# Performance work log

Measured on AMD Instinct MI355X. Metric: run time of the kernel, lower is better.

Reference implementation:

```python
import jax, jax.numpy as jnp
import numpy as np

N_NODES = 100000
N_EDGES = 1600000
N_GRAPHS = 1000
F_IN, HID = 9, 64


def _glorot(key, shape):
    fan_in, fan_out = shape[0], shape[1]
    lim = (6.0 / (fan_in + fan_out)) ** 0.5
    return jax.random.uniform(key, shape, jnp.float32, -lim, lim)


def setup_inputs() -> dict:
    key = jax.random.key(0)
    ks = jax.random.split(key, 12)
    x = jax.random.normal(ks[0], (N_NODES, F_IN), jnp.float32)
    edge_index = jax.random.randint(ks[1], (2, N_EDGES), 0, N_NODES, jnp.int64)
    edge_attr = jnp.zeros((N_EDGES, 1), jnp.float32)
    batch = jnp.sort(jax.random.randint(ks[2], (N_NODES,), 0, N_GRAPHS, jnp.int64))
    # SAGEConv layer 1: 9 -> 64 (lin_l on aggregated neighbors w/ bias, lin_r on root)
    Wl1 = _glorot(ks[3], (F_IN, HID)); Wr1 = _glorot(ks[4], (F_IN, HID)); b1 = jnp.zeros((HID,), jnp.float32)
    # SAGEConv layer 2: 64 -> 64
    Wl2 = _glorot(ks[5], (HID, HID)); Wr2 = _glorot(ks[6], (HID, HID)); b2 = jnp.zeros((HID,), jnp.float32)
    # MLP readout: 64 -> 32 -> 1
    Wm1 = _glorot(ks[7], (HID, HID // 2)); bm1 = jnp.zeros((HID // 2,), jnp.float32)
    Wm2 = _glorot(ks[8], (HID // 2, 1)); bm2 = jnp.zeros((1,), jnp.float32)
    return dict(x=x, edge_index=edge_index, edge_attr=edge_attr, batch=batch,
                Wl1=Wl1, Wr1=Wr1, b1=b1, Wl2=Wl2, Wr2=Wr2, b2=b2,
                Wm1=Wm1, bm1=bm1, Wm2=Wm2, bm2=bm2)


def _sage_conv(x, src, dst, Wl, Wr, b, n_nodes):
    # mean aggregation of source-node features onto target nodes
    msgs = x[src]                                              # [E, F] gather
    s = jax.ops.segment_sum(msgs, dst, num_segments=n_nodes)   # [N, F] scatter-add
    cnt = jax.ops.segment_sum(jnp.ones((src.shape[0],), x.dtype), dst, num_segments=n_nodes)
    agg = s / jnp.maximum(cnt, 1.0)[:, None]
    return agg @ Wl + x @ Wr + b


def reference(x, edge_index, edge_attr, batch,
              Wl1, Wr1, b1, Wl2, Wr2, b2, Wm1, bm1, Wm2, bm2):
    src, dst = edge_index[0], edge_index[1]
    n = x.shape[0]
    h = jax.nn.relu(_sage_conv(x, src, dst, Wl1, Wr1, b1, n))
    h = _sage_conv(h, src, dst, Wl2, Wr2, b2, n)               # no act after last layer
    # global mean pool over graphs
    gs = jax.ops.segment_sum(h, batch, num_segments=N_GRAPHS)
    gc = jax.ops.segment_sum(jnp.ones((n,), h.dtype), batch, num_segments=N_GRAPHS)
    xg = gs / jnp.maximum(gc, 1.0)[:, None]                    # [G, 64]
    out = jax.nn.sigmoid(jax.nn.relu(xg @ Wm1 + bm1) @ Wm2 + bm2)  # [G, 1]
    return out
```

## Files before the change

### kernel.cpp

```cpp
#include <hip/hip_runtime.h>
#include <math.h>

#define N_NODES  100000
#define N_EDGES  1600000
#define N_GRAPHS 1000
#define F_IN     9
#define HID      64
#define NBUCK    196
#define BCAP     12288
#define CHUNK    4096

typedef unsigned int uint32;
typedef float v2f __attribute__((ext_vector_type(2)));


__device__ __forceinline__ uint32 pk_lo(float a, float b, uint32 old) {
    return (uint32)__builtin_amdgcn_cvt_pk_fp8_f32(a, b, (int)old, false);
}
__device__ __forceinline__ uint32 pk_hi(float a, float b, uint32 old) {
    return (uint32)__builtin_amdgcn_cvt_pk_fp8_f32(a, b, (int)old, true);
}

__global__ __launch_bounds__(256) void pad_part_kernel(const float* __restrict__ x,
                                                       const int* __restrict__ ei,
                                                       int* __restrict__ gcur,
                                                       int* __restrict__ ebuf,
                                                       uint32* __restrict__ x8b) {
    __shared__ int lcnt[NBUCK], lbase[NBUCK];
    int tid = threadIdx.x;

    int n = blockIdx.x * 256 + tid;
    if (n < N_NODES) {
        uint32 w[4];
        #pragma unroll
        for (int p = 0; p < 4; ++p) {
            float v0 = (4 * p + 0 < F_IN) ? x[(size_t)n * F_IN + 4 * p + 0] : 0.0f;
            float v1 = (4 * p + 1 < F_IN) ? x[(size_t)n * F_IN + 4 * p + 1] : 0.0f;
            float v2 = (4 * p + 2 < F_IN) ? x[(size_t)n * F_IN + 4 * p + 2] : 0.0f;
            float v3 = (4 * p + 3 < F_IN) ? x[(size_t)n * F_IN + 4 * p + 3] : 0.0f;
            w[p] = pk_hi(v2, v3, pk_lo(v0, v1, 0u));
        }
        *reinterpret_cast<uint4*>(&x8b[(size_t)n * 4]) =
            make_uint4(w[0], w[1], w[2], w[3]);
    }

    for (int i = tid; i < NBUCK; i += 256) lcnt[i] = 0;
    __syncthreads();
    int e0 = blockIdx.x * CHUNK;
    int e1 = e0 + CHUNK; if (e1 > N_EDGES) e1 = N_EDGES;
    for (int e = e0 + tid; e < e1; e += 256)
        atomicAdd(&lcnt[ei[N_EDGES + e] >> 9], 1);
    __syncthreads();
    for (int i = tid; i < NBUCK; i += 256)
        lbase[i] = atomicAdd(&gcur[i], lcnt[i]);
    __syncthreads();
    for (int i = tid; i < NBUCK; i += 256) lcnt[i] = 0;
    __syncthreads();
    for (int e = e0 + tid; e < e1; e += 256) {
        int src = ei[e];
        int dst = ei[N_EDGES + e];
        int b = dst >> 9;
        int pos = lbase[b] + atomicAdd(&lcnt[b], 1);
        if (pos < BCAP)
            ebuf[(size_t)b * BCAP + pos] = src | ((dst & 511) << 17);
    }
}

__global__ __launch_bounds__(512) void build_csr_kernel(const int* __restrict__ ebuf,
                                                        const int* __restrict__ gcur,
                                                        int2* __restrict__ rowcnt,
                                                        int* __restrict__ col) {
    __shared__ int cnt[512];
    __shared__ int cur[512];
    __shared__ int wsum[8];
    int b = blockIdx.x;
    int n0 = b << 9;
    int tid = threadIdx.x;
    int ec = gcur[b]; if (ec > BCAP) ec = BCAP;
    size_t base = (size_t)b * BCAP;
    cnt[tid] = 0;
    __syncthreads();
    for (int e = tid; e < ec; e += 512)
        atomicAdd(&cnt[(uint32)ebuf[base + e] >> 17], 1);
    __syncthreads();
    int v = cnt[tid];
    int lane = tid & 63, wid = tid >> 6;
    int s = v;
    #pragma unroll
    for (int off = 1; off < 64; off <<= 1) {
        int u = __shfl_up(s, off, 64);
        if (lane >= off) s += u;
    }
    if (lane == 63) wsum[wid] = s;
    __syncthreads();
    int add = 0;
    for (int w = 0; w < wid; ++w) add += wsum[w];
    int off_ex = s - v + add;
    int n = n0 + tid;
    if (n < N_NODES) rowcnt[n] = make_int2((int)base + off_ex, v);
    cur[tid] = off_ex;
    __syncthreads();
    for (int e = tid; e < ec; e += 512) {
        int pv = ebuf[base + e];
        int pos = atomicAdd(&cur[(uint32)pv >> 17], 1);
        col[base + pos] = pv & 0x1FFFF;
    }
}

__global__ __launch_bounds__(256) void agg_l1_kernel(const float* __restrict__ x,
                                                     const uint32* __restrict__ x8b,
                                                     const int2* __restrict__ rowcnt,
                                                     const int* __restrict__ col,
                                                     const float* __restrict__ Wl1,
                                                     const float* __restrict__ Wr1,
                                                     const float* __restrict__ b1,
                                                     const int* __restrict__ batch,
                                                     uint32* __restrict__ h1b,
                                                     float* __restrict__ poolH) {
    __shared__ float w1s[F_IN * 128];
    __shared__ float bs[HID];
    __shared__ float ss[64 * 17];
    __shared__ float xs[64 * 10];
    __shared__ float hs[64 * 65];
    int tid = threadIdx.x;
    int n0 = blockIdx.x * 64;
    for (int i = tid; i < F_IN * HID; i += 256) {
        int f = i >> 6, j = i & 63;
        w1s[f * 128 + j]      = Wl1[i];
        w1s[f * 128 + 64 + j] = Wr1[i];
    }
    if (tid < HID) bs[tid] = b1[tid];
    for (int i = tid; i < 64 * F_IN; i += 256) {
        int r = i / F_IN, f = i - r * F_IN;
        int n = n0 + r;
        xs[r * 10 + f] = (n < N_NODES) ? x[(size_t)n * F_IN + f] : 0.0f;
    }

    {
        int r = tid >> 2, q = tid & 3;
        int n = n0 + r;
        v2f a01 = {0.f, 0.f}, a23 = {0.f, 0.f};
        int deg = 0;
        if (n < N_NODES) {
            int2 rc = rowcnt[n];
            deg = rc.y;
            int i = 0;
            for (; i + 1 < deg; i += 2) {
                int c0 = col[rc.x + i];
                int c1 = col[rc.x + i + 1];
                uint32 d0 = x8b[(size_t)c0 * 4 + q];
                uint32 d1 = x8b[(size_t)c1 * 4 + q];
                a01 += __builtin_amdgcn_cvt_pk_f32_fp8((int)d0, false);
                a23 += __builtin_amdgcn_cvt_pk_f32_fp8((int)d0, true);
                a01 += __builtin_amdgcn_cvt_pk_f32_fp8((int)d1, false);
                a23 += __builtin_amdgcn_cvt_pk_f32_fp8((int)d1, true);
            }
            if (i < deg) {
                uint32 d0 = x8b[(size_t)col[rc.x + i] * 4 + q];
                a01 += __builtin_amdgcn_cvt_pk_f32_fp8((int)d0, false);
                a23 += __builtin_amdgcn_cvt_pk_f32_fp8((int)d0, true);
            }
        }
        float inv = 1.0f / fmaxf((float)deg, 1.0f);
        int q4 = q * 4;
        ss[r * 17 + q4 + 0] = a01[0] * inv;
        ss[r * 17 + q4 + 1] = a01[1] * inv;
        ss[r * 17 + q4 + 2] = a23[0] * inv;
        ss[r * 17 + q4 + 3] = a23[1] * inv;
    }
    __syncthreads();

    int r = tid >> 2, cg = tid & 3, k0 = cg * 16;
    float h[16];
    #pragma unroll
    for (int kk = 0; kk < 16; ++kk) {
        int k = k0 + kk;
        float v = bs[k];
        #pragma unroll
        for (int f = 0; f < F_IN; ++f)
            v += ss[r * 17 + f] * w1s[f * 128 + k]
               + xs[r * 10 + f] * w1s[f * 128 + 64 + k];
        v = fmaxf(v, 0.0f);
        h[kk] = v;
        hs[r * 65 + k] = v;
    }
    int n = n0 + r;
    if (n < N_NODES) {
        uint32 w[4];
        #pragma unroll
        for (int p = 0; p < 4; ++p)
            w[p] = pk_hi(h[4 * p + 2], h[4 * p + 3],
                         pk_lo(h[4 * p + 0], h[4 * p + 1], 0u));
        *reinterpret_cast<uint4*>(&h1b[(size_t)n * 16 + cg * 4]) =
            make_uint4(w[0], w[1], w[2], w[3]);
    }
    __syncthreads();
    if (tid < HID) {
        int j = tid;
        int cur = batch[(n0 < N_NODES) ? n0 : (N_NODES - 1)];
        float v = (n0 < N_NODES) ? hs[0 * 65 + j] : 0.0f;
        for (int rr = 1; rr < 64; ++rr) {
            int nn = n0 + rr;
            bool ok = (nn < N_NODES);
            int g = batch[ok ? nn : (N_NODES - 1)];
            float val = ok ? hs[rr * 65 + j] : 0.0f;
            if (g == cur) v += val;
            else { atomicAdd(&poolH[cur * HID + j], v); cur = g; v = val; }
        }
        atomicAdd(&poolH[cur * HID + j], v);
    }
}

__global__ __launch_bounds__(256) void gather2_kernel(const uint32* __restrict__ h1b,
                                                      const int2* __restrict__ rowcnt,
                                                      const int* __restrict__ col,
                                                      const int* __restrict__ batch,
                                                      float* __restrict__ poolA) {
    __shared__ float sh[4][HID];
    int w = threadIdx.x >> 6;
    int lane = threadIdx.x & 63;
    int slot = lane >> 3;
    int grp  = lane & 7;
    int n = blockIdx.x * 4 + w;
    int2 rc = rowcnt[n];
    const uint32* hb = h1b + grp * 2;
    v2f a0 = {0.f, 0.f}, a1 = {0.f, 0.f}, a2 = {0.f, 0.f}, a3 = {0.f, 0.f};
    int i = rc.x + slot;
    int end = rc.x + rc.y;
    for (; i + 8 < end; i += 16) {
        int c0 = col[i];
        int c1 = col[i + 8];
        uint2 d0 = *reinterpret_cast<const uint2*>(hb + (size_t)c0 * 16);
        uint2 d1 = *reinterpret_cast<const uint2*>(hb + (size_t)c1 * 16);
        a0 += __builtin_amdgcn_cvt_pk_f32_fp8((int)d0.x, false);
        a1 += __builtin_amdgcn_cvt_pk_f32_fp8((int)d0.x, true);
        a2 += __builtin_amdgcn_cvt_pk_f32_fp8((int)d0.y, false);
        a3 += __builtin_amdgcn_cvt_pk_f32_fp8((int)d0.y, true);
        a0 += __builtin_amdgcn_cvt_pk_f32_fp8((int)d1.x, false);
        a1 += __builtin_amdgcn_cvt_pk_f32_fp8((int)d1.x, true);
        a2 += __builtin_amdgcn_cvt_pk_f32_fp8((int)d1.y, false);
        a3 += __builtin_amdgcn_cvt_pk_f32_fp8((int)d1.y, true);
    }
    if (i < end) {
        int c0 = col[i];
        uint2 d0 = *reinterpret_cast<const uint2*>(hb + (size_t)c0 * 16);
        a0 += __builtin_amdgcn_cvt_pk_f32_fp8((int)d0.x, false);
        a1 += __builtin_amdgcn_cvt_pk_f32_fp8((int)d0.x, true);
        a2 += __builtin_amdgcn_cvt_pk_f32_fp8((int)d0.y, false);
        a3 += __builtin_amdgcn_cvt_pk_f32_fp8((int)d0.y, true);
    }
    float r8[8] = {a0[0], a0[1], a1[0], a1[1], a2[0], a2[1], a3[0], a3[1]};
    #pragma unroll
    for (int k = 0; k < 8; ++k) {
        r8[k] += __shfl_xor(r8[k], 8, 64);
        r8[k] += __shfl_xor(r8[k], 16, 64);
        r8[k] += __shfl_xor(r8[k], 32, 64);
    }
    float inv = 1.0f / fmaxf((float)rc.y, 1.0f);
    if (slot == 0) {
        #pragma unroll
        for (int k = 0; k < 8; ++k)
            sh[w][grp * 8 + k] = r8[k] * inv;
    }
    __syncthreads();
    if (threadIdx.x < HID) {
        int j = threadIdx.x;
        int base = blockIdx.x * 4;
        int cur = batch[base];
        float v = sh[0][j];
        #pragma unroll
        for (int r = 1; r < 4; ++r) {
            int g = batch[base + r];
            float val = sh[r][j];
            if (g == cur) v += val;
            else { atomicAdd(&poolA[cur * HID + j], v); cur = g; v = val; }
        }
        atomicAdd(&poolA[cur * HID + j], v);
    }
}

__global__ void mlp_kernel(const float* __restrict__ poolA,
                           const float* __restrict__ poolH,
                           const int* __restrict__ batch,
                           const float* __restrict__ Wl2,
                           const float* __restrict__ Wr2,
                           const float* __restrict__ b2,
                           const float* __restrict__ Wm1,
                           const float* __restrict__ bm1,
                           const float* __restrict__ Wm2,
                           const float* __restrict__ bm2,
                           float* __restrict__ out) {
    __shared__ float spA[4][HID], spH[4][HID], sx[4][HID];
    int t = blockIdx.x * blockDim.x + threadIdx.x;
    int g = t >> 6;
    int j = t & 63;
    int w = threadIdx.x >> 6;
    if (g >= N_GRAPHS) return;
    int lo = 0, hi = N_NODES;
    while (lo < hi) { int m = (lo + hi) >> 1; if (batch[m] < g) lo = m + 1; else hi = m; }
    int start = lo;
    lo = 0; hi = N_NODES;
    while (lo < hi) { int m = (lo + hi) >> 1; if (batch[m] < g + 1) lo = m + 1; else hi = m; }
    int cntg = lo - start;
    float inv = 1.0f / fmaxf((float)cntg, 1.0f);
    spA[w][j] = poolA[g * HID + j];
    spH[w][j] = poolH[g * HID + j];
    float acc = 0.0f;
    #pragma unroll 8
    for (int k = 0; k < HID; ++k)
        acc += spA[w][k] * Wl2[k * HID + j] + spH[w][k] * Wr2[k * HID + j];
    sx[w][j] = acc * inv + b2[j];
    if (j < 32) {
        float a = bm1[j];
        #pragma unroll 8
        for (int k = 0; k < HID; ++k)
            a += sx[w][k] * Wm1[k * 32 + j];
        float r = fmaxf(a, 0.0f) * Wm2[j];
        #pragma unroll
        for (int off = 16; off > 0; off >>= 1)
            r += __shfl_down(r, off, 32);
        if (j == 0)
            out[g] = 1.0f / (1.0f + expf(-(r + bm2[0])));
    }
}

extern "C" void kernel_launch(void* const* d_in, const int* in_sizes, int n_in,
                              void* d_out, int out_size, void* d_ws, size_t ws_size,
                              hipStream_t stream) {
    const float* x    = (const float*)d_in[0];
    const int*   ei   = (const int*)d_in[1];
    const int*   batch= (const int*)d_in[3];
    const float* Wl1  = (const float*)d_in[4];
    const float* Wr1  = (const float*)d_in[5];
    const float* b1   = (const float*)d_in[6];
    const float* Wl2  = (const float*)d_in[7];
    const float* Wr2  = (const float*)d_in[8];
    const float* b2   = (const float*)d_in[9];
    const float* Wm1  = (const float*)d_in[10];
    const float* bm1  = (const float*)d_in[11];
    const float* Wm2  = (const float*)d_in[12];
    const float* bm2  = (const float*)d_in[13];
    float* out = (float*)d_out;

    int*   wsi = (int*)d_ws;
    float* wsf = (float*)d_ws;
    float*  poolA  = wsf;
    float*  poolH  = wsf + 64000;
    int*    gcur   = wsi + 128000;
    int2*   rowcnt = (int2*)(wsi + 128200);
    int*    col    = wsi + 328200;
    int*    ebuf   = wsi + 2736648;
    uint32* x8b    = (uint32*)(wsi + 5145096);
    uint32* h1b    = (uint32*)(wsi + 5545096);

    hipMemsetAsync(d_ws, 0, 128200 * sizeof(int), stream);

    {   int bl = (N_EDGES + CHUNK - 1) / CHUNK;
        pad_part_kernel<<<bl, 256, 0, stream>>>(x, ei, gcur, ebuf, x8b);
    }
    build_csr_kernel<<<NBUCK, 512, 0, stream>>>(ebuf, gcur, rowcnt, col);
    {   int th = 256, bl = (N_NODES + 63) / 64;
        agg_l1_kernel<<<bl, th, 0, stream>>>(x, x8b, rowcnt, col, Wl1, Wr1, b1,
                                             batch, h1b, poolH);
    }
    {   int th = 256, bl = N_NODES / 4;
        gather2_kernel<<<bl, th, 0, stream>>>(h1b, rowcnt, col, batch, poolA);
    }
    {   int th = 256, bl = (N_GRAPHS * 64) / th;
        mlp_kernel<<<bl, th, 0, stream>>>(poolA, poolH, batch,
                                          Wl2, Wr2, b2, Wm1, bm1, Wm2, bm2, out);
    }
}
```

Baseline: 139.4 us.

## Split layer-1 gather into wave-per-node kernel and halve CSR bucket size

The layer-1 neighbour gather moves out of the fused aggregation kernel into a separate kernel. There, one 64-lane wave handles each node, 16 slots stride over its edges and a shuffle reduction combines them, writing mean features to a new s16 buffer. The dense layer-1 kernel then only loads those sums. CSR construction buckets become 256 nodes instead of 512, doubling the number of build blocks for more parallelism, with the workspace layout adjusted. The cost is an extra launch and an extra round trip of the intermediate buffer through global memory. Halving bucket capacity to 6144 raises the risk of overflow on skewed inputs.

Result: slower. 152.9 us (+9.7%).

```diff
diff --git a/kernel.cpp b/kernel.cpp
--- a/kernel.cpp
+++ b/kernel.cpp
@@ -6,8 +6,8 @@
 #define N_GRAPHS 1000
 #define F_IN     9
 #define HID      64
-#define NBUCK    196
-#define BCAP     12288
+#define NBUCK    391
+#define BCAP     6144
 #define CHUNK    4096
 
 typedef unsigned int uint32;
@@ -49,7 +49,7 @@
     int e0 = blockIdx.x * CHUNK;
     int e1 = e0 + CHUNK; if (e1 > N_EDGES) e1 = N_EDGES;
     for (int e = e0 + tid; e < e1; e += 256)
-        atomicAdd(&lcnt[ei[N_EDGES + e] >> 9], 1);
+        atomicAdd(&lcnt[ei[N_EDGES + e] >> 8], 1);
     __syncthreads();
     for (int i = tid; i < NBUCK; i += 256)
         lbase[i] = atomicAdd(&gcur[i], lcnt[i]);
@@ -59,10 +59,10 @@
     for (int e = e0 + tid; e < e1; e += 256) {
         int src = ei[e];
         int dst = ei[N_EDGES + e];
-        int b = dst >> 9;
+        int b = dst >> 8;
         int pos = lbase[b] + atomicAdd(&lcnt[b], 1);
         if (pos < BCAP)
-            ebuf[(size_t)b * BCAP + pos] = src | ((dst & 511) << 17);
+            ebuf[(size_t)b * BCAP + pos] = src | ((dst & 255) << 17);
     }
 }
 
@@ -70,35 +70,40 @@
                                                         const int* __restrict__ gcur,
                                                         int2* __restrict__ rowcnt,
                                                         int* __restrict__ col) {
-    __shared__ int cnt[512];
-    __shared__ int cur[512];
-    __shared__ int wsum[8];
+    __shared__ int cnt[256];
+    __shared__ int cur[256];
+    __shared__ int wsum[4];
     int b = blockIdx.x;
-    int n0 = b << 9;
+    int n0 = b << 8;
     int tid = threadIdx.x;
     int ec = gcur[b]; if (ec > BCAP) ec = BCAP;
     size_t base = (size_t)b * BCAP;
-    cnt[tid] = 0;
+    if (tid < 256) cnt[tid] = 0;
     __syncthreads();
     for (int e = tid; e < ec; e += 512)
         atomicAdd(&cnt[(uint32)ebuf[base + e] >> 17], 1);
     __syncthreads();
-    int v = cnt[tid];
+    int v = 0, s = 0;
     int lane = tid & 63, wid = tid >> 6;
-    int s = v;
-    #pragma unroll
-    for (int off = 1; off < 64; off <<= 1) {
-        int u = __shfl_up(s, off, 64);
-        if (lane >= off) s += u;
-    }
-    if (lane == 63) wsum[wid] = s;
-    __syncthreads();
-    int add = 0;
-    for (int w = 0; w < wid; ++w) add += wsum[w];
-    int off_ex = s - v + add;
-    int n = n0 + tid;
-    if (n < N_NODES) rowcnt[n] = make_int2((int)base + off_ex, v);
-    cur[tid] = off_ex;
+    if (tid < 256) {
+        v = cnt[tid];
+        s = v;
+        #pragma unroll
+        for (int off = 1; off < 64; off <<= 1) {
+            int u = __shfl_up(s, off, 64);
+            if (lane >= off) s += u;
+        }
+        if (lane == 63) wsum[wid] = s;
+    }
+    __syncthreads();
+    if (tid < 256) {
+        int add = 0;
+        for (int w = 0; w < wid; ++w) add += wsum[w];
+        int off_ex = s - v + add;
+        int n = n0 + tid;
+        if (n < N_NODES) rowcnt[n] = make_int2((int)base + off_ex, v);
+        cur[tid] = off_ex;
+    }
     __syncthreads();
     for (int e = tid; e < ec; e += 512) {
         int pv = ebuf[base + e];
@@ -107,16 +112,46 @@
     }
 }
 
-__global__ __launch_bounds__(256) void agg_l1_kernel(const float* __restrict__ x,
-                                                     const uint32* __restrict__ x8b,
-                                                     const int2* __restrict__ rowcnt,
-                                                     const int* __restrict__ col,
-                                                     const float* __restrict__ Wl1,
-                                                     const float* __restrict__ Wr1,
-                                                     const float* __restrict__ b1,
-                                                     const int* __restrict__ batch,
-                                                     uint32* __restrict__ h1b,
-                                                     float* __restrict__ poolH) {
+__global__ __launch_bounds__(256) void gather1_kernel(const uint32* __restrict__ x8b,
+                                                      const int2* __restrict__ rowcnt,
+                                                      const int* __restrict__ col,
+                                                      float* __restrict__ s16) {
+    int w = threadIdx.x >> 6;
+    int lane = threadIdx.x & 63;
+    int slot = lane >> 2;
+    int q    = lane & 3;
+    int n = blockIdx.x * 4 + w;
+    int2 rc = rowcnt[n];
+    v2f a01 = {0.f, 0.f}, a23 = {0.f, 0.f};
+    for (int i = slot; i < rc.y; i += 16) {
+        int c = col[rc.x + i];
+        uint32 d = x8b[(size_t)c * 4 + q];
+        a01 += __builtin_amdgcn_cvt_pk_f32_fp8((int)d, false);
+        a23 += __builtin_amdgcn_cvt_pk_f32_fp8((int)d, true);
+    }
+    float r4[4] = {a01[0], a01[1], a23[0], a23[1]};
+    #pragma unroll
+    for (int k = 0; k < 4; ++k) {
+        r4[k] += __shfl_xor(r4[k], 4, 64);
+        r4[k] += __shfl_xor(r4[k], 8, 64);
+        r4[k] += __shfl_xor(r4[k], 16, 64);
+        r4[k] += __shfl_xor(r4[k], 32, 64);
+    }
+    if (slot == 0) {
+        float inv = 1.0f / fmaxf((float)rc.y, 1.0f);
+        *reinterpret_cast<float4*>(&s16[(size_t)n * 16 + q * 4]) =
+            make_float4(r4[0] * inv, r4[1] * inv, r4[2] * inv, r4[3] * inv);
+    }
+}
+
+__global__ __launch_bounds__(256) void l1_kernel(const float* __restrict__ x,
+                                                 const float* __restrict__ s16,
+                                                 const float* __restrict__ Wl1,
+                                                 const float* __restrict__ Wr1,
+                                                 const float* __restrict__ b1,
+                                                 const int* __restrict__ batch,
+                                                 uint32* __restrict__ h1b,
+                                                 float* __restrict__ poolH) {
     __shared__ float w1s[F_IN * 128];
     __shared__ float bs[HID];
     __shared__ float ss[64 * 17];
@@ -130,43 +165,15 @@
         w1s[f * 128 + 64 + j] = Wr1[i];
     }
     if (tid < HID) bs[tid] = b1[tid];
+    for (int i = tid; i < 64 * 16; i += 256) {
+        int r = i >> 4, f = i & 15;
+        int n = n0 + r;
+        ss[r * 17 + f] = (n < N_NODES) ? s16[(size_t)n * 16 + f] : 0.0f;
+    }
     for (int i = tid; i < 64 * F_IN; i += 256) {
         int r = i / F_IN, f = i - r * F_IN;
         int n = n0 + r;
         xs[r * 10 + f] = (n < N_NODES) ? x[(size_t)n * F_IN + f] : 0.0f;
-    }
-
-    {
-        int r = tid >> 2, q = tid & 3;
-        int n = n0 + r;
-        v2f a01 = {0.f, 0.f}, a23 = {0.f, 0.f};
-        int deg = 0;
-        if (n < N_NODES) {
-            int2 rc = rowcnt[n];
-            deg = rc.y;
-            int i = 0;
-            for (; i + 1 < deg; i += 2) {
-                int c0 = col[rc.x + i];
-                int c1 = col[rc.x + i + 1];
-                uint32 d0 = x8b[(size_t)c0 * 4 + q];
-                uint32 d1 = x8b[(size_t)c1 * 4 + q];
-                a01 += __builtin_amdgcn_cvt_pk_f32_fp8((int)d0, false);
-                a23 += __builtin_amdgcn_cvt_pk_f32_fp8((int)d0, true);
-                a01 += __builtin_amdgcn_cvt_pk_f32_fp8((int)d1, false);
-                a23 += __builtin_amdgcn_cvt_pk_f32_fp8((int)d1, true);
-            }
-            if (i < deg) {
-                uint32 d0 = x8b[(size_t)col[rc.x + i] * 4 + q];
-                a01 += __builtin_amdgcn_cvt_pk_f32_fp8((int)d0, false);
-                a23 += __builtin_amdgcn_cvt_pk_f32_fp8((int)d0, true);
-            }
-        }
-        float inv = 1.0f / fmaxf((float)deg, 1.0f);
-        int q4 = q * 4;
-        ss[r * 17 + q4 + 0] = a01[0] * inv;
-        ss[r * 17 + q4 + 1] = a01[1] * inv;
-        ss[r * 17 + q4 + 2] = a23[0] * inv;
-        ss[r * 17 + q4 + 3] = a23[1] * inv;
     }
     __syncthreads();
 
@@ -347,21 +354,24 @@
     float*  poolA  = wsf;
     float*  poolH  = wsf + 64000;
     int*    gcur   = wsi + 128000;
-    int2*   rowcnt = (int2*)(wsi + 128200);
-    int*    col    = wsi + 328200;
-    int*    ebuf   = wsi + 2736648;
-    uint32* x8b    = (uint32*)(wsi + 5145096);
-    uint32* h1b    = (uint32*)(wsi + 5545096);
-
-    hipMemsetAsync(d_ws, 0, 128200 * sizeof(int), stream);
+    int2*   rowcnt = (int2*)(wsi + 128400);
+    int*    col    = wsi + 328400;
+    int*    ebuf   = wsi + 2730704;
+    uint32* x8b    = (uint32*)(wsi + 5133008);
+    float*  s16    = wsf + 5533008;
+    uint32* h1b    = (uint32*)(wsi + 7133008);
+
+    hipMemsetAsync(d_ws, 0, 128400 * sizeof(int), stream);
 
     {   int bl = (N_EDGES + CHUNK - 1) / CHUNK;
         pad_part_kernel<<<bl, 256, 0, stream>>>(x, ei, gcur, ebuf, x8b);
     }
     build_csr_kernel<<<NBUCK, 512, 0, stream>>>(ebuf, gcur, rowcnt, col);
+    {   int th = 256, bl = N_NODES / 4;
+        gather1_kernel<<<bl, th, 0, stream>>>(x8b, rowcnt, col, s16);
+    }
     {   int th = 256, bl = (N_NODES + 63) / 64;
-        agg_l1_kernel<<<bl, th, 0, stream>>>(x, x8b, rowcnt, col, Wl1, Wr1, b1,
-                                             batch, h1b, poolH);
+        l1_kernel<<<bl, th, 0, stream>>>(x, s16, Wl1, Wr1, b1, batch, h1b, poolH);
     }
     {   int th = 256, bl = N_NODES / 4;
         gather2_kernel<<<bl, th, 0, stream>>>(h1b, rowcnt, col, batch, poolA);
```
